# Performance work log

Measured on AMD Instinct MI355X. Metric: run time of the kernel, lower is better.

The kernel has to match this reference:

```python
import jax, jax.numpy as jnp
import numpy as np
from jax import lax

L1_DECAY = 1e-06


def _maxpool2(x):
    # NCHW 2x2 max pool, stride 2
    return lax.reduce_window(x, -jnp.inf, lax.max, (1, 1, 2, 2), (1, 1, 2, 2), 'VALID')


def _cnn(x, w1, b1, w2, b2, wo, bo):
    # x: [N,128,128] -> [N,64], z-score normalized over batch dim
    x = x[:, None]  # [N,1,128,128]
    dn = ('NCHW', 'OIHW', 'NCHW')
    x = lax.conv_general_dilated(x, w1, (1, 1), 'SAME', dimension_numbers=dn) + b1[None, :, None, None]
    x = _maxpool2(jax.nn.relu(x))  # [N,4,64,64]
    x = lax.conv_general_dilated(x, w2, (1, 1), 'SAME', dimension_numbers=dn) + b2[None, :, None, None]
    x = _maxpool2(jax.nn.relu(x))  # [N,8,32,32]
    x = x.reshape(x.shape[0], -1)  # [N,8192] (C,H,W order, as torch .view)
    x = x @ wo.T + bo  # [N,64]
    mean = x.mean(axis=0)
    std = x.std(axis=0, ddof=1)  # torch unbiased std
    return (x - mean) / std


def _interact(item, nbr):
    # item: [N,64]; nbr: [N,H,K,64]. dot-attention over K per node/hop.
    scores = jnp.einsum('nhkd,nd->nhk', nbr, item)
    attn = jax.nn.softmax(scores, axis=-1)
    return jnp.einsum('nhk,nhkd->nhd', attn, nbr)  # [N,H,64]


def setup_inputs() -> dict:
    key = jax.random.key(0)
    ks = jax.random.split(key, 16)
    B = 4096
    inp = {}
    inp['data'] = jax.random.randint(ks[0], (B, 3), 0, 76)
    inp['cell_nbr'] = jax.random.randint(ks[1], (76, 2, 128), 0, 15970)
    inp['drug_nbr'] = jax.random.randint(ks[2], (764, 2, 128), 0, 15970)
    inp['protein_table'] = jax.random.normal(ks[3], (15970, 64), jnp.float32)
    inp['cell_emb_pre'] = jax.random.normal(ks[4], (76, 128, 128), jnp.float32)
    inp['drug_emb_pre'] = jax.random.normal(ks[5], (764, 128, 128), jnp.float32)
    inp['conv1_w'] = 0.05 * jax.random.normal(ks[6], (4, 1, 3, 3), jnp.float32)
    inp['conv1_b'] = 0.05 * jax.random.normal(ks[7], (4,), jnp.float32)
    inp['conv2_w'] = 0.05 * jax.random.normal(ks[8], (8, 4, 3, 3), jnp.float32)
    inp['conv2_b'] = 0.05 * jax.random.normal(ks[9], (8,), jnp.float32)
    inp['out_w'] = 0.05 * jax.random.normal(ks[10], (64, 8192), jnp.float32)
    inp['out_b'] = 0.05 * jax.random.normal(ks[11], (64,), jnp.float32)
    inp['agg_w'] = 0.05 * jax.random.normal(ks[12], (64, 128), jnp.float32)
    inp['agg_b'] = 0.05 * jax.random.normal(ks[13], (64,), jnp.float32)
    inp['comb_w'] = 0.05 * jax.random.normal(ks[14], (64, 128), jnp.float32)
    return inp


def reference(data, cell_nbr, drug_nbr, protein_table, cell_emb_pre, drug_emb_pre,
              conv1_w, conv1_b, conv2_w, conv2_b, out_w, out_b, agg_w, agg_b, comb_w):
    cells, drug1, drug2 = data[:, 0], data[:, 1], data[:, 2]
    B = data.shape[0]

    # per-node neighbor embedding gather: [num, n_hop, K, 64]
    cell_nbr_emb = protein_table[cell_nbr]
    drug_nbr_emb = protein_table[drug_nbr]

    # CNN item embeddings from precomputed images
    cell_item = _cnn(cell_emb_pre, conv1_w, conv1_b, conv2_w, conv2_b, out_w, out_b)  # [76,64]
    drug_item = _cnn(drug_emb_pre, conv1_w, conv1_b, conv2_w, conv2_b, out_w, out_b)  # [764,64]

    # gather -> attend -> weighted sum, then concat hops and aggregate
    cell_i = _interact(cell_item, cell_nbr_emb).reshape(cell_item.shape[0], -1)  # [76,128]
    drug_i = _interact(drug_item, drug_nbr_emb).reshape(drug_item.shape[0], -1)  # [764,128]
    cell_emb = cell_i @ agg_w.T + agg_b  # [76,64]
    drug_emb = drug_i @ agg_w.T + agg_b  # [764,64]

    # batch gather, keep singleton dim 1 to match torch stacking of [1,64]
    ce = cell_emb[cells][:, None, :]   # [B,1,64]
    d1e = drug_emb[drug1][:, None, :]
    d2e = drug_emb[drug2][:, None, :]

    # therapy: transformation_matrix
    combined = jnp.concatenate([d1e, d2e], axis=2) @ comb_w.T  # [B,1,64]
    therapy = (combined * ce).sum(axis=2)  # [B,1]
    toxic = (d1e * d2e).sum(axis=2)        # [B,1]
    score = therapy - toxic

    # emb loss (faithful to source: neighbor lists are indexed on the BATCH dim by hop)
    cnl = cell_nbr_emb[cells]   # [B,2,128,64]
    dnl1 = drug_nbr_emb[drug1]
    dnl2 = drug_nbr_emb[drug2]
    sq = lambda t: jnp.sum(t * t)
    item_reg = (sq(ce) + sq(d1e) + sq(d2e)) / 2
    node_reg = jnp.float32(0.0)
    for hop in range(2):
        node_reg = node_reg + (sq(cnl[hop]) + sq(dnl1[hop]) + sq(dnl2[hop])) / 2
    emb_loss = L1_DECAY * (item_reg + node_reg) / B
    return score, emb_loss
```

## Files before the change

### kernel.cpp

```cpp
#include <hip/hip_runtime.h>
#include <hip/hip_bf16.h>
#include <math.h>

#define N_CELL 76
#define N_DRUG 764
#define N_ITEM 840
#define BATCH  4096

#define POOL2H_B 0u
#define POOL2L_B 13762560u
#define WHI_B    27525120u
#define WLO_B    28573696u
#define XFC_B    29622272u
#define ITEM_B   29837312u
#define EMB_B    30052352u
#define V_B      30267392u
#define LOSS_B   30306304u
#define CNT_B    30306368u
#define FRAG_B   30306432u

typedef short bh8 __attribute__((ext_vector_type(8)));
typedef short bh4 __attribute__((ext_vector_type(4)));
typedef float f32x4 __attribute__((ext_vector_type(4)));

static __device__ inline unsigned short f2bf(float f) {
  union { float f; unsigned u; } v; v.f = f;
  unsigned r = v.u + 0x7FFFu + ((v.u >> 16) & 1u);
  return (unsigned short)(r >> 16);
}
static __device__ inline float bf2f(unsigned short h) {
  union { unsigned u; float f; } v; v.u = ((unsigned)h) << 16;
  return v.f;
}
static __device__ inline unsigned short f2bf_lo(float f, unsigned short h) {
  union { float f; unsigned u; } a; a.f = f - bf2f(h);
  return (unsigned short)(a.u >> 16);
}
static __device__ inline unsigned cvtpk(float a, float b) {
  unsigned r;
  asm("v_cvt_pk_bf16_f32 %0, %1, %2" : "=v"(r) : "v"(a), "v"(b));
  return r;
}
static __device__ inline float fromu(unsigned u) {
  union { unsigned u; float f; } v; v.u = u; return v.f;
}
static __device__ inline unsigned asu(float f) {
  union { float f; unsigned u; } v; v.f = f; return v.u;
}

union BH8U { bh8 v; struct { bh4 lo, hi; } s; };

__global__ __launch_bounds__(64) void k_prep(
    const float* __restrict__ w1, const float* __restrict__ w2,
    const float* __restrict__ b2, bh8* __restrict__ ftab,
    float* __restrict__ loss, unsigned* __restrict__ cnt) {
  int lane = threadIdx.x & 63;
  int ml = lane & 15, q = lane >> 4;
  int oc = ml & 3, yv1 = (ml >> 2) & 1, hi = ml >> 3;
  bh8 BhE, BlE, BhO, BlO;
  {
    int kr = q - yv1;
    bool krok = (kr >= 0 && kr <= 2);
#pragma unroll
    for (int j = 0; j < 8; ++j) {
      float ve = 0.f, vo = 0.f;
      if (krok) {
        int kse = j - 3 - 2 * hi;
        int kso = j - 2 * hi;
        if (kse >= 0 && kse <= 2) ve = w1[oc * 9 + kr * 3 + kse];
        if (kso >= 0 && kso <= 2) vo = w1[oc * 9 + kr * 3 + kso];
      }
      unsigned short he = f2bf(ve), ho = f2bf(vo);
      BhE[j] = (short)he; BlE[j] = (short)f2bf_lo(ve, he);
      BhO[j] = (short)ho; BlO[j] = (short)f2bf_lo(vo, ho);
    }
  }
  int oc_b = ml & 7, yv2 = ml >> 3;
  bh8 Bh2[2], Bl2[2];
#pragma unroll
  for (int ch = 0; ch < 2; ++ch) {
#pragma unroll
    for (int j = 0; j < 8; ++j) {
      int kg = ch * 32 + q * 8 + j;
      float v = 0.f;
      if (kg < 48) {
        int r = kg / 12, rem = kg - r * 12;
        int ks = rem >> 2, ic = rem & 3;
        int kr = r - yv2;
        if (kr >= 0 && kr <= 2) v = w2[(oc_b * 4 + ic) * 9 + kr * 3 + ks];
      } else if (kg == 48) {
        v = b2[oc_b];
      }
      unsigned short h = f2bf(v);
      Bh2[ch][j] = (short)h;
      Bl2[ch][j] = (short)f2bf_lo(v, h);
    }
  }
  ftab[lane] = BhE;          ftab[64 + lane] = BlE;
  ftab[128 + lane] = BhO;    ftab[192 + lane] = BlO;
  ftab[256 + lane] = Bh2[0]; ftab[320 + lane] = Bl2[0];
  ftab[384 + lane] = Bh2[1]; ftab[448 + lane] = Bl2[1];
  if (lane == 0) { *loss = 0.f; *cnt = 0u; }
}

__global__ __launch_bounds__(512) void k_conv12(
    const float* __restrict__ cell_pre, const float* __restrict__ drug_pre,
    const float* __restrict__ b1, const float* __restrict__ out_w,
    const bh8* __restrict__ ftab,
    unsigned short* __restrict__ pool2h, unsigned short* __restrict__ pool2l,
    unsigned short* __restrict__ whi, unsigned short* __restrict__ wlo,
    float* __restrict__ xfc) {
  __shared__ unsigned short slh[38 * 34 * 4];
  __shared__ unsigned short sll[38 * 34 * 4];
  __shared__ unsigned short p1h[18 * 66 * 4];
  __shared__ unsigned short p1l[18 * 66 * 4];
  int n = blockIdx.y;
  int tid = threadIdx.x;
  if (n >= 840) {
    int cb = (n - 840) * 4 + blockIdx.x;
    int gid = cb * 512 + tid;
    for (int i = gid; i < 13440; i += 10240)
      ((float4*)xfc)[i] = make_float4(0.f, 0.f, 0.f, 0.f);
    for (int i = gid; i < 131072; i += 10240) {
      float4 v = ((const float4*)out_w)[i];
      unsigned h01 = cvtpk(v.x, v.y), h23 = cvtpk(v.z, v.w);
      float d0 = v.x - fromu(h01 << 16), d1 = v.y - fromu(h01 & 0xFFFF0000u);
      float d2 = v.z - fromu(h23 << 16), d3 = v.w - fromu(h23 & 0xFFFF0000u);
      uint2 hh; hh.x = h01; hh.y = h23;
      uint2 lw; lw.x = cvtpk(d0, d1); lw.y = cvtpk(d2, d3);
      ((uint2*)whi)[i] = hh;
      ((uint2*)wlo)[i] = lw;
    }
    return;
  }
  int qt = blockIdx.x;
  const float4* src = (const float4*)((n < N_CELL) ? (cell_pre + (size_t)n * 16384)
                                                   : (drug_pre + (size_t)(n - N_CELL) * 16384));
  for (int i = tid; i < 38 * 32; i += 512) {
    int lr = i >> 5, g = i & 31;
    int iy = qt * 32 - 3 + lr;
    float4 v = make_float4(0.f, 0.f, 0.f, 0.f);
    if (iy >= 0 && iy < 128) v = src[iy * 32 + g];
    unsigned h01 = cvtpk(v.x, v.y), h23 = cvtpk(v.z, v.w);
    unsigned l01 = (asu(v.x - fromu(h01 << 16)) >> 16) |
                   (asu(v.y - fromu(h01 & 0xFFFF0000u)) & 0xFFFF0000u);
    unsigned l23 = (asu(v.z - fromu(h23 << 16)) >> 16) |
                   (asu(v.w - fromu(h23 & 0xFFFF0000u)) & 0xFFFF0000u);
    uint2 hh; hh.x = h01; hh.y = h23;
    uint2 lw; lw.x = l01; lw.y = l23;
    ((uint2*)slh)[lr * 34 + g + 1] = hh;
    ((uint2*)sll)[lr * 34 + g + 1] = lw;
  }
  if (tid < 76) {
    int lr = tid >> 1, g = (tid & 1) ? 33 : 0;
    ushort4 z = make_ushort4(0, 0, 0, 0);
    ((ushort4*)slh)[lr * 34 + g] = z;
    ((ushort4*)sll)[lr * 34 + g] = z;
  }
  if (tid < 36) {
    int r = tid >> 1, c = (tid & 1) ? 65 : 0;
    ushort4 z = make_ushort4(0, 0, 0, 0);
    ((ushort4*)p1h)[r * 66 + c] = z;
    ((ushort4*)p1l)[r * 66 + c] = z;
  }
  int wv = tid >> 6;
  int lane = tid & 63;
  int ml = lane & 15, q = lane >> 4;
  int oc = ml & 3, yv1 = (ml >> 2) & 1, hi = ml >> 3;
  int oc_b = ml & 7, yv2 = ml >> 3;
  float bb = b1[oc];

  bh8 BhE = ftab[lane],        BlE = ftab[64 + lane];
  bh8 BhO = ftab[128 + lane],  BlO = ftab[192 + lane];
  bh8 Bh20 = ftab[256 + lane], Bl20 = ftab[320 + lane];
  bh8 Bh21 = ftab[384 + lane], Bl21 = ftab[448 + lane];

  int c0 = 2 * q, c1 = 2 * q + 1;
  int c2 = 8 + 2 * q, c3 = 9 + 2 * q;
  if (c2 > 11) { c2 = 8; c3 = 9; }
  int r0 = (c0 * 86) >> 8, s0 = c0 - 3 * r0;
  int r1 = (c1 * 86) >> 8, s1 = c1 - 3 * r1;
  int r2 = (c2 * 86) >> 8, s2 = c2 - 3 * r2;
  int r3 = (c3 * 86) >> 8, s3 = c3 - 3 * r3;
  int x2 = (wv & 3) << 4;
  int off0 = r0 * 66 + x2 + ml + s0;
  int off1 = r1 * 66 + x2 + ml + s1;
  int off2 = r2 * 66 + x2 + ml + s2;
  int off3 = r3 * 66 + x2 + ml + s3;
  __syncthreads();

  int x0 = (wv & 1) * 16;
  int g1 = wv >> 1;
  int rbase = (g1 < 2) ? g1 * 5 : 10 + (g1 - 2) * 4;
  int rcnt  = (g1 < 2) ? 5 : 4;
  int Lb = x0 + ml;
  const bh4* lh4 = (const bh4*)slh;
  const bh4* ll4 = (const bh4*)sll;
#pragma unroll 1
  for (int ii = 0; ii < rcnt; ++ii) {
    int i = rbase + ii;
    int base = (2 * i + q) * 34 + Lb;
    bh4 g0h = lh4[base], g1h = lh4[base + 1], g2h = lh4[base + 2];
    bh4 g0l = ll4[base], g1l = ll4[base + 1], g2l = ll4[base + 2];
    BH8U aeh, ael, aoh, aol;
    aeh.s.lo = g0h; aeh.s.hi = g1h;
    ael.s.lo = g0l; ael.s.hi = g1l;
    aoh.s.lo = g1h; aoh.s.hi = g2h;
    aol.s.lo = g1l; aol.s.hi = g2l;
    f32x4 de = {0.f, 0.f, 0.f, 0.f}, dd = de;
    de = __builtin_amdgcn_mfma_f32_16x16x32_bf16(aeh.v, BhE, de, 0, 0, 0);
    de = __builtin_amdgcn_mfma_f32_16x16x32_bf16(aeh.v, BlE, de, 0, 0, 0);
    de = __builtin_amdgcn_mfma_f32_16x16x32_bf16(ael.v, BhE, de, 0, 0, 0);
    dd = __builtin_amdgcn_mfma_f32_16x16x32_bf16(aoh.v, BhO, dd, 0, 0, 0);
    dd = __builtin_amdgcn_mfma_f32_16x16x32_bf16(aoh.v, BlO, dd, 0, 0, 0);
    dd = __builtin_amdgcn_mfma_f32_16x16x32_bf16(aol.v, BhO, dd, 0, 0, 0);
    int pr = qt * 16 - 1 + i;
    bool inr = (pr >= 0 && pr < 64);
    float t, t2, v0, v1, v2, v3;
    t = fmaxf(de[0], dd[0]); t2 = __shfl_xor(t, 4); v0 = fmaxf(fmaxf(t, t2) + bb, 0.f);
    t = fmaxf(de[1], dd[1]); t2 = __shfl_xor(t, 4); v1 = fmaxf(fmaxf(t, t2) + bb, 0.f);
    t = fmaxf(de[2], dd[2]); t2 = __shfl_xor(t, 4); v2 = fmaxf(fmaxf(t, t2) + bb, 0.f);
    t = fmaxf(de[3], dd[3]); t2 = __shfl_xor(t, 4); v3 = fmaxf(fmaxf(t, t2) + bb, 0.f);
    if (yv1 == 0) {
      if (!inr) { v0 = 0.f; v1 = 0.f; v2 = 0.f; v3 = 0.f; }
      unsigned pk01 = cvtpk(v0, v1), pk23 = cvtpk(v2, v3);
      unsigned l0 = asu(v0 - fromu(pk01 << 16)) >> 16;
      unsigned l1 = asu(v1 - fromu(pk01 & 0xFFFF0000u)) >> 16;
      unsigned l2 = asu(v2 - fromu(pk23 << 16)) >> 16;
      unsigned l3 = asu(v3 - fromu(pk23 & 0xFFFF0000u)) >> 16;
      int idx = (i * 66 + 2 * (x0 + q * 4) + hi + 1) * 4 + oc;
      p1h[idx] = (unsigned short)pk01;              p1l[idx] = (unsigned short)l0;
      p1h[idx + 8] = (unsigned short)(pk01 >> 16);  p1l[idx + 8] = (unsigned short)l1;
      p1h[idx + 16] = (unsigned short)pk23;         p1l[idx + 16] = (unsigned short)l2;
      p1h[idx + 24] = (unsigned short)(pk23 >> 16); p1l[idx + 24] = (unsigned short)l3;
    }
  }
  __syncthreads();

  int rp0 = (wv >> 2) * 4;
  const bh4* ph4 = (const bh4*)p1h;
  const bh4* pl4 = (const bh4*)p1l;
#pragma unroll 1
  for (int rr = 0; rr < 4; ++rr) {
    int rp = rp0 + rr;
    int base2 = 2 * rp * 66;
    BH8U ah0, al0, ah1, al1;
    ah0.s.lo = ph4[base2 + off0]; ah0.s.hi = ph4[base2 + off1];
    al0.s.lo = pl4[base2 + off0]; al0.s.hi = pl4[base2 + off1];
    if (q < 2) {
      ah1.s.lo = ph4[base2 + off2]; ah1.s.hi = ph4[base2 + off3];
      al1.s.lo = pl4[base2 + off2]; al1.s.hi = pl4[base2 + off3];
    } else {
#pragma unroll
      for (int j = 0; j < 8; ++j) { ah1.v[j] = 0; al1.v[j] = 0; }
      if (q == 2) ah1.v[0] = (short)0x3F80;
    }
    f32x4 accA = {0.f, 0.f, 0.f, 0.f}, accB = accA;
    accA = __builtin_amdgcn_mfma_f32_16x16x32_bf16(ah0.v, Bh20, accA, 0, 0, 0);
    accA = __builtin_amdgcn_mfma_f32_16x16x32_bf16(ah0.v, Bl20, accA, 0, 0, 0);
    accA = __builtin_amdgcn_mfma_f32_16x16x32_bf16(al0.v, Bh20, accA, 0, 0, 0);
    accB = __builtin_amdgcn_mfma_f32_16x16x32_bf16(ah1.v, Bh21, accB, 0, 0, 0);
    accB = __builtin_amdgcn_mfma_f32_16x16x32_bf16(ah1.v, Bl21, accB, 0, 0, 0);
    accB = __builtin_amdgcn_mfma_f32_16x16x32_bf16(al1.v, Bh21, accB, 0, 0, 0);
    float d0 = accA[0] + accB[0], d1 = accA[1] + accB[1];
    float d2 = accA[2] + accB[2], d3 = accA[3] + accB[3];
    float m0 = fmaxf(d0, d1), m1 = fmaxf(d2, d3);
    float o0 = __shfl_xor(m0, 8), o1 = __shfl_xor(m1, 8);
    m0 = fmaxf(fmaxf(m0, o0), 0.f);
    m1 = fmaxf(fmaxf(m1, o1), 0.f);
    if (yv2 == 0) {
      unsigned pk = cvtpk(m0, m1);
      float e0 = m0 - fromu(pk << 16), e1 = m1 - fromu(pk & 0xFFFF0000u);
      unsigned lw = cvtpk(e0, e1);
      int PR = qt * 8 + rp;
      unsigned ui = (unsigned)n * 4096u + (unsigned)oc_b * 512u +
                    (unsigned)PR * 16u + (unsigned)(x2 >> 2) + (unsigned)q;
      ((unsigned*)pool2h)[ui] = pk;
      ((unsigned*)pool2l)[ui] = lw;
    }
  }
}

__global__ __launch_bounds__(512) void k_fc(
    const unsigned short* __restrict__ pool2h, const unsigned short* __restrict__ pool2l,
    const unsigned short* __restrict__ whi, const unsigned short* __restrict__ wlo,
    float* __restrict__ xfc) {
  __shared__ float buf[8][1104];
  int mt = blockIdx.x, kc4 = blockIdx.y;
  int tid = threadIdx.x;
  int wv = tid >> 6;
  int lane = tid & 63;
  int ml = lane & 15, q = lane >> 4;
  int row = mt * 16 + ml; if (row > N_ITEM - 1) row = N_ITEM - 1;
  size_t k0 = ((size_t)kc4 * 8 + wv) * 256 + q * 8;
  const bh8* Ah = (const bh8*)(pool2h + (size_t)row * 8192 + k0);
  const bh8* Al = (const bh8*)(pool2l + (size_t)row * 8192 + k0);
  const bh8* Bh[4], * Bl[4];
#pragma unroll
  for (int nb = 0; nb < 4; ++nb) {
    Bh[nb] = (const bh8*)(whi + (size_t)(nb * 16 + ml) * 8192 + k0);
    Bl[nb] = (const bh8*)(wlo + (size_t)(nb * 16 + ml) * 8192 + k0);
  }
  f32x4 acc[4];
#pragma unroll
  for (int nb = 0; nb < 4; ++nb) acc[nb] = (f32x4){0.f, 0.f, 0.f, 0.f};
#pragma unroll
  for (int st = 0; st < 8; ++st) {
    bh8 ah = Ah[st * 4], al = Al[st * 4];
#pragma unroll
    for (int nb = 0; nb < 4; ++nb) {
      bh8 bhv = Bh[nb][st * 4], blv = Bl[nb][st * 4];
      acc[nb] = __builtin_amdgcn_mfma_f32_16x16x32_bf16(ah, bhv, acc[nb], 0, 0, 0);
      acc[nb] = __builtin_amdgcn_mfma_f32_16x16x32_bf16(ah, blv, acc[nb], 0, 0, 0);
      acc[nb] = __builtin_amdgcn_mfma_f32_16x16x32_bf16(al, bhv, acc[nb], 0, 0, 0);
    }
  }
  {
    float* bw = &buf[wv][lane * 17];
#pragma unroll
    for (int nb = 0; nb < 4; ++nb)
#pragma unroll
      for (int r = 0; r < 4; ++r) bw[nb * 4 + r] = acc[nb][r];
  }
  __syncthreads();
#pragma unroll
  for (int su = 0; su < 2; ++su) {
    int s = tid + su * 512;
    int ln = s >> 4, j = s & 15;
    int phys = ln * 17 + j;
    float v = buf[0][phys] + buf[1][phys] + buf[2][phys] + buf[3][phys] +
              buf[4][phys] + buf[5][phys] + buf[6][phys] + buf[7][phys];
    int nb = j >> 2, r = j & 3;
    int mml = ln & 15, mq = ln >> 4;
    int mr = mt * 16 + mq * 4 + r;
    if (mr < N_ITEM) atomicAdd(xfc + (size_t)mr * 64 + nb * 16 + mml, v);
  }
}

__global__ __launch_bounds__(256) void k_norm(
    const float* __restrict__ xfc, float* __restrict__ item) {
  __shared__ float red[256];
  int grp = blockIdx.x >> 6;
  int o = blockIdx.x & 63;
  int base = grp ? N_CELL : 0;
  int N = grp ? N_DRUG : N_CELL;
  int tid = threadIdx.x;
  float s = 0.f;
  for (int i = tid; i < N; i += 256) s += xfc[(size_t)(base + i) * 64 + o];
  red[tid] = s; __syncthreads();
  for (int w = 128; w > 0; w >>= 1) { if (tid < w) red[tid] += red[tid + w]; __syncthreads(); }
  float mean = red[0] / (float)N;
  __syncthreads();
  float sq = 0.f;
  for (int i = tid; i < N; i += 256) {
    float d = xfc[(size_t)(base + i) * 64 + o] - mean;
    sq += d * d;
  }
  red[tid] = sq; __syncthreads();
  for (int w = 128; w > 0; w >>= 1) { if (tid < w) red[tid] += red[tid + w]; __syncthreads(); }
  float inv_std = 1.f / sqrtf(red[0] / (float)(N - 1));
  for (int i = tid; i < N; i += 256)
    item[(size_t)(base + i) * 64 + o] = (xfc[(size_t)(base + i) * 64 + o] - mean) * inv_std;
}

__global__ __launch_bounds__(512) void k_interact(
    const int* __restrict__ cell_nbr, const int* __restrict__ drug_nbr,
    const float* __restrict__ protein, const float* __restrict__ item,
    const float* __restrict__ agg_w, const float* __restrict__ agg_b,
    const float* __restrict__ comb_w, float* __restrict__ emb,
    float* __restrict__ V) {
  __shared__ float pb[2][128 * 65];
  __shared__ float item_s[64];
  __shared__ float sc[2][128];
  __shared__ float hop_out[128];
  __shared__ float red[512];
  __shared__ float emb_f[64];
  int n = blockIdx.x;
  int tid = threadIdx.x;
  int ht = tid >> 8;
  int t = tid & 255;
  const int* nbr = (n < N_CELL) ? (cell_nbr + (size_t)n * 256)
                                : (drug_nbr + (size_t)(n - N_CELL) * 256);
  if (tid < 64) item_s[tid] = item[(size_t)n * 64 + tid];
  __syncthreads();
  for (int e = t; e < 8192; e += 256) {
    int k = e >> 6, d = e & 63;
    int idx = nbr[ht * 128 + k];
    pb[ht][k * 65 + d] = protein[(size_t)idx * 64 + d];
  }
  __syncthreads();
  {
    int k = t >> 1, halfd = t & 1;
    int d0 = halfd * 32;
    float p = 0.f;
#pragma unroll
    for (int d = 0; d < 32; ++d) p += item_s[d0 + d] * pb[ht][k * 65 + d0 + d];
    p += __shfl_xor(p, 1);
    if (halfd == 0) sc[ht][k] = p;
  }
  __syncthreads();
  if (t < 64) {
    float a = sc[ht][t], b = sc[ht][t + 64];
    float m = fmaxf(a, b);
#pragma unroll
    for (int off = 32; off > 0; off >>= 1) m = fmaxf(m, __shfl_xor(m, off));
    float e0 = __expf(a - m), e1 = __expf(b - m);
    float s = e0 + e1;
#pragma unroll
    for (int off = 32; off > 0; off >>= 1) s += __shfl_xor(s, off);
    float inv = 1.f / s;
    sc[ht][t] = e0 * inv; sc[ht][t + 64] = e1 * inv;
  }
  __syncthreads();
  {
    int d = t & 63, kq = t >> 6;
    float p = 0.f;
#pragma unroll
    for (int k = 0; k < 32; ++k) {
      int kk = kq * 32 + k;
      p += sc[ht][kk] * pb[ht][kk * 65 + d];
    }
    red[tid] = p;
  }
  __syncthreads();
  if (t < 64)
    hop_out[ht * 64 + t] = red[ht * 256 + t] + red[ht * 256 + t + 64] +
                           red[ht * 256 + t + 128] + red[ht * 256 + t + 192];
  __syncthreads();
  {
    int o = tid & 63, jq = tid >> 6;
    float p = 0.f;
#pragma unroll
    for (int j = 0; j < 16; ++j) {
      int jj = jq * 16 + j;
      p += hop_out[jj] * agg_w[(size_t)o * 128 + jj];
    }
    red[tid] = p;
  }
  __syncthreads();
  if (tid < 64) {
    float ev = red[tid] + red[tid + 64] + red[tid + 128] + red[tid + 192] +
               red[tid + 256] + red[tid + 320] + red[tid + 384] + red[tid + 448] +
               agg_b[tid];
    emb[(size_t)n * 64 + tid] = ev;
    emb_f[tid] = ev;
  }
  if (n < N_CELL) {
    __syncthreads();
    if (tid < 128) {
      float s = 0.f;
#pragma unroll
      for (int o = 0; o < 64; ++o) s += comb_w[(size_t)o * 128 + tid] * emb_f[o];
      V[(size_t)n * 128 + tid] = s;
    }
  }
}

__global__ __launch_bounds__(512) void k_scoreall(
    const int* __restrict__ data, const int* __restrict__ cell_nbr,
    const int* __restrict__ drug_nbr, const float* __restrict__ protein,
    const float* __restrict__ emb, const float* __restrict__ V,
    float* __restrict__ out, float* __restrict__ loss, unsigned* __restrict__ cnt) {
  __shared__ float red[8];
  int bx = blockIdx.x;
  int tid = threadIdx.x;
  int lane = tid & 63;
  int wv = tid >> 6;
  float part = 0.f;
  if (bx < 64) {
    int b0 = bx * 64 + wv * 8;
#pragma unroll 1
    for (int i = 0; i < 8; ++i) {
      int b = b0 + i;
      int c = data[b * 3 + 0], d1 = data[b * 3 + 1], d2 = data[b * 3 + 2];
      float ce = emb[(size_t)c * 64 + lane];
      float e1 = emb[(size_t)(N_CELL + d1) * 64 + lane];
      float e2 = emb[(size_t)(N_CELL + d2) * 64 + lane];
      float v1 = V[(size_t)c * 128 + lane];
      float v2 = V[(size_t)c * 128 + 64 + lane];
      float s = e1 * v1 + e2 * v2 - e1 * e2;
      part += ce * ce + e1 * e1 + e2 * e2;
#pragma unroll
      for (int off = 32; off > 0; off >>= 1) s += __shfl_xor(s, off);
      if (lane == 0) out[b] = s;
    }
  } else {
    int j = bx - 64;
    int hop = j / 3, which = j % 3;
    int row = data[hop * 3 + which];
    const int* nbr = (which == 0) ? (cell_nbr + (size_t)row * 256)
                                  : (drug_nbr + (size_t)row * 256);
    for (int e = tid; e < 16384; e += 512) {
      int k = e >> 6, d = e & 63;
      float v = protein[(size_t)nbr[k] * 64 + d];
      part += v * v;
    }
  }
#pragma unroll
  for (int off = 32; off > 0; off >>= 1) part += __shfl_xor(part, off);
  if (lane == 0) red[wv] = part;
  __syncthreads();
  if (tid == 0) {
    float s = red[0] + red[1] + red[2] + red[3] + red[4] + red[5] + red[6] + red[7];
    atomicAdd(loss, 0.5f * s);
    __threadfence();
    unsigned old = atomicAdd(cnt, 1u);
    if (old == gridDim.x - 1) {
      float L = atomicAdd(loss, 0.f);
      out[BATCH] = L * (1e-6f / 4096.f);
    }
  }
}

extern "C" void kernel_launch(void* const* d_in, const int* in_sizes, int n_in,
                              void* d_out, int out_size, void* d_ws, size_t ws_size,
                              hipStream_t stream) {
  const int*   data      = (const int*)d_in[0];
  const int*   cell_nbr  = (const int*)d_in[1];
  const int*   drug_nbr  = (const int*)d_in[2];
  const float* protein   = (const float*)d_in[3];
  const float* cell_pre  = (const float*)d_in[4];
  const float* drug_pre  = (const float*)d_in[5];
  const float* w1        = (const float*)d_in[6];
  const float* b1        = (const float*)d_in[7];
  const float* w2        = (const float*)d_in[8];
  const float* b2        = (const float*)d_in[9];
  const float* out_w     = (const float*)d_in[10];
  const float* agg_w     = (const float*)d_in[12];
  const float* agg_b     = (const float*)d_in[13];
  const float* comb_w    = (const float*)d_in[14];
  float* out = (float*)d_out;
  char* base = (char*)d_ws;
  unsigned short* pool2h  = (unsigned short*)(base + POOL2H_B);
  unsigned short* pool2l  = (unsigned short*)(base + POOL2L_B);
  unsigned short* whi     = (unsigned short*)(base + WHI_B);
  unsigned short* wlo     = (unsigned short*)(base + WLO_B);
  float* xfc              = (float*)(base + XFC_B);
  float* item             = (float*)(base + ITEM_B);
  float* emb              = (float*)(base + EMB_B);
  float* V                = (float*)(base + V_B);
  float* loss             = (float*)(base + LOSS_B);
  unsigned* cnt           = (unsigned*)(base + CNT_B);
  bh8* ftab               = (bh8*)(base + FRAG_B);

  k_prep<<<1, 64, 0, stream>>>(w1, w2, b2, ftab, loss, cnt);
  k_conv12<<<dim3(4, 845), 512, 0, stream>>>(cell_pre, drug_pre, b1, out_w, ftab,
                                             pool2h, pool2l, whi, wlo, xfc);
  k_fc<<<dim3(53, 4), 512, 0, stream>>>(pool2h, pool2l, whi, wlo, xfc);
  k_norm<<<128, 256, 0, stream>>>(xfc, item);
  k_interact<<<840, 512, 0, stream>>>(cell_nbr, drug_nbr, protein, item, agg_w, agg_b,
                                      comb_w, emb, V);
  k_scoreall<<<70, 512, 0, stream>>>(data, cell_nbr, drug_nbr, protein, emb, V, out, loss, cnt);
}
```

Before: 211.2 us.

## Process all four row-quarters per block with register-prefetched next halo tile

The conv kernel now launches one block per item instead of four, looping over the four 32-row quarters inside the block. While conv2 of the current quarter runs, the global loads for the next quarter's input tile are issued into registers and written to shared memory afterwards, so load latency overlaps compute. This cuts the grid from 3380 to 845 blocks, which reduces parallelism and may hurt latency hiding, but it removes per-block launch overhead and one redundant halo reload. It adds extra barriers and register pressure from the prefetched float4 values.

```diff
diff --git a/kernel.cpp b/kernel.cpp
--- a/kernel.cpp
+++ b/kernel.cpp
@@ -114,14 +114,13 @@
   __shared__ unsigned short sll[38 * 34 * 4];
   __shared__ unsigned short p1h[18 * 66 * 4];
   __shared__ unsigned short p1l[18 * 66 * 4];
-  int n = blockIdx.y;
+  int n = blockIdx.x;
   int tid = threadIdx.x;
   if (n >= 840) {
-    int cb = (n - 840) * 4 + blockIdx.x;
-    int gid = cb * 512 + tid;
-    for (int i = gid; i < 13440; i += 10240)
+    int gid = (n - 840) * 512 + tid;
+    for (int i = gid; i < 13440; i += 2560)
       ((float4*)xfc)[i] = make_float4(0.f, 0.f, 0.f, 0.f);
-    for (int i = gid; i < 131072; i += 10240) {
+    for (int i = gid; i < 131072; i += 2560) {
       float4 v = ((const float4*)out_w)[i];
       unsigned h01 = cvtpk(v.x, v.y), h23 = cvtpk(v.z, v.w);
       float d0 = v.x - fromu(h01 << 16), d1 = v.y - fromu(h01 & 0xFFFF0000u);
@@ -133,24 +132,8 @@
     }
     return;
   }
-  int qt = blockIdx.x;
   const float4* src = (const float4*)((n < N_CELL) ? (cell_pre + (size_t)n * 16384)
                                                    : (drug_pre + (size_t)(n - N_CELL) * 16384));
-  for (int i = tid; i < 38 * 32; i += 512) {
-    int lr = i >> 5, g = i & 31;
-    int iy = qt * 32 - 3 + lr;
-    float4 v = make_float4(0.f, 0.f, 0.f, 0.f);
-    if (iy >= 0 && iy < 128) v = src[iy * 32 + g];
-    unsigned h01 = cvtpk(v.x, v.y), h23 = cvtpk(v.z, v.w);
-    unsigned l01 = (asu(v.x - fromu(h01 << 16)) >> 16) |
-                   (asu(v.y - fromu(h01 & 0xFFFF0000u)) & 0xFFFF0000u);
-    unsigned l23 = (asu(v.z - fromu(h23 << 16)) >> 16) |
-                   (asu(v.w - fromu(h23 & 0xFFFF0000u)) & 0xFFFF0000u);
-    uint2 hh; hh.x = h01; hh.y = h23;
-    uint2 lw; lw.x = l01; lw.y = l23;
-    ((uint2*)slh)[lr * 34 + g + 1] = hh;
-    ((uint2*)sll)[lr * 34 + g + 1] = lw;
-  }
   if (tid < 76) {
     int lr = tid >> 1, g = (tid & 1) ? 33 : 0;
     ushort4 z = make_ushort4(0, 0, 0, 0);
@@ -187,96 +170,157 @@
   int off1 = r1 * 66 + x2 + ml + s1;
   int off2 = r2 * 66 + x2 + ml + s2;
   int off3 = r3 * 66 + x2 + ml + s3;
-  __syncthreads();
-
   int x0 = (wv & 1) * 16;
   int g1 = wv >> 1;
   int rbase = (g1 < 2) ? g1 * 5 : 10 + (g1 - 2) * 4;
   int rcnt  = (g1 < 2) ? 5 : 4;
   int Lb = x0 + ml;
+  int rp0 = (wv >> 2) * 4;
   const bh4* lh4 = (const bh4*)slh;
   const bh4* ll4 = (const bh4*)sll;
-#pragma unroll 1
-  for (int ii = 0; ii < rcnt; ++ii) {
-    int i = rbase + ii;
-    int base = (2 * i + q) * 34 + Lb;
-    bh4 g0h = lh4[base], g1h = lh4[base + 1], g2h = lh4[base + 2];
-    bh4 g0l = ll4[base], g1l = ll4[base + 1], g2l = ll4[base + 2];
-    BH8U aeh, ael, aoh, aol;
-    aeh.s.lo = g0h; aeh.s.hi = g1h;
-    ael.s.lo = g0l; ael.s.hi = g1l;
-    aoh.s.lo = g1h; aoh.s.hi = g2h;
-    aol.s.lo = g1l; aol.s.hi = g2l;
-    f32x4 de = {0.f, 0.f, 0.f, 0.f}, dd = de;
-    de = __builtin_amdgcn_mfma_f32_16x16x32_bf16(aeh.v, BhE, de, 0, 0, 0);
-    de = __builtin_amdgcn_mfma_f32_16x16x32_bf16(aeh.v, BlE, de, 0, 0, 0);
-    de = __builtin_amdgcn_mfma_f32_16x16x32_bf16(ael.v, BhE, de, 0, 0, 0);
-    dd = __builtin_amdgcn_mfma_f32_16x16x32_bf16(aoh.v, BhO, dd, 0, 0, 0);
-    dd = __builtin_amdgcn_mfma_f32_16x16x32_bf16(aoh.v, BlO, dd, 0, 0, 0);
-    dd = __builtin_amdgcn_mfma_f32_16x16x32_bf16(aol.v, BhO, dd, 0, 0, 0);
-    int pr = qt * 16 - 1 + i;
-    bool inr = (pr >= 0 && pr < 64);
-    float t, t2, v0, v1, v2, v3;
-    t = fmaxf(de[0], dd[0]); t2 = __shfl_xor(t, 4); v0 = fmaxf(fmaxf(t, t2) + bb, 0.f);
-    t = fmaxf(de[1], dd[1]); t2 = __shfl_xor(t, 4); v1 = fmaxf(fmaxf(t, t2) + bb, 0.f);
-    t = fmaxf(de[2], dd[2]); t2 = __shfl_xor(t, 4); v2 = fmaxf(fmaxf(t, t2) + bb, 0.f);
-    t = fmaxf(de[3], dd[3]); t2 = __shfl_xor(t, 4); v3 = fmaxf(fmaxf(t, t2) + bb, 0.f);
-    if (yv1 == 0) {
-      if (!inr) { v0 = 0.f; v1 = 0.f; v2 = 0.f; v3 = 0.f; }
-      unsigned pk01 = cvtpk(v0, v1), pk23 = cvtpk(v2, v3);
-      unsigned l0 = asu(v0 - fromu(pk01 << 16)) >> 16;
-      unsigned l1 = asu(v1 - fromu(pk01 & 0xFFFF0000u)) >> 16;
-      unsigned l2 = asu(v2 - fromu(pk23 << 16)) >> 16;
-      unsigned l3 = asu(v3 - fromu(pk23 & 0xFFFF0000u)) >> 16;
-      int idx = (i * 66 + 2 * (x0 + q * 4) + hi + 1) * 4 + oc;
-      p1h[idx] = (unsigned short)pk01;              p1l[idx] = (unsigned short)l0;
-      p1h[idx + 8] = (unsigned short)(pk01 >> 16);  p1l[idx + 8] = (unsigned short)l1;
-      p1h[idx + 16] = (unsigned short)pk23;         p1l[idx + 16] = (unsigned short)l2;
-      p1h[idx + 24] = (unsigned short)(pk23 >> 16); p1l[idx + 24] = (unsigned short)l3;
-    }
-  }
-  __syncthreads();
-
-  int rp0 = (wv >> 2) * 4;
   const bh4* ph4 = (const bh4*)p1h;
   const bh4* pl4 = (const bh4*)p1l;
+  int si0 = tid, si1 = tid + 512, si2 = tid + 1024;
+  bool sk2 = (si2 < 1216);
+
+  for (int i = tid; i < 1216; i += 512) {
+    int lr = i >> 5, g = i & 31;
+    int iy = -3 + lr;
+    float4 v = make_float4(0.f, 0.f, 0.f, 0.f);
+    if (iy >= 0 && iy < 128) v = src[iy * 32 + g];
+    unsigned h01 = cvtpk(v.x, v.y), h23 = cvtpk(v.z, v.w);
+    unsigned l01 = (asu(v.x - fromu(h01 << 16)) >> 16) |
+                   (asu(v.y - fromu(h01 & 0xFFFF0000u)) & 0xFFFF0000u);
+    unsigned l23 = (asu(v.z - fromu(h23 << 16)) >> 16) |
+                   (asu(v.w - fromu(h23 & 0xFFFF0000u)) & 0xFFFF0000u);
+    uint2 hh; hh.x = h01; hh.y = h23;
+    uint2 lw; lw.x = l01; lw.y = l23;
+    ((uint2*)slh)[lr * 34 + g + 1] = hh;
+    ((uint2*)sll)[lr * 34 + g + 1] = lw;
+  }
+  __syncthreads();
+
 #pragma unroll 1
-  for (int rr = 0; rr < 4; ++rr) {
-    int rp = rp0 + rr;
-    int base2 = 2 * rp * 66;
-    BH8U ah0, al0, ah1, al1;
-    ah0.s.lo = ph4[base2 + off0]; ah0.s.hi = ph4[base2 + off1];
-    al0.s.lo = pl4[base2 + off0]; al0.s.hi = pl4[base2 + off1];
-    if (q < 2) {
-      ah1.s.lo = ph4[base2 + off2]; ah1.s.hi = ph4[base2 + off3];
-      al1.s.lo = pl4[base2 + off2]; al1.s.hi = pl4[base2 + off3];
-    } else {
-#pragma unroll
-      for (int j = 0; j < 8; ++j) { ah1.v[j] = 0; al1.v[j] = 0; }
-      if (q == 2) ah1.v[0] = (short)0x3F80;
-    }
-    f32x4 accA = {0.f, 0.f, 0.f, 0.f}, accB = accA;
-    accA = __builtin_amdgcn_mfma_f32_16x16x32_bf16(ah0.v, Bh20, accA, 0, 0, 0);
-    accA = __builtin_amdgcn_mfma_f32_16x16x32_bf16(ah0.v, Bl20, accA, 0, 0, 0);
-    accA = __builtin_amdgcn_mfma_f32_16x16x32_bf16(al0.v, Bh20, accA, 0, 0, 0);
-    accB = __builtin_amdgcn_mfma_f32_16x16x32_bf16(ah1.v, Bh21, accB, 0, 0, 0);
-    accB = __builtin_amdgcn_mfma_f32_16x16x32_bf16(ah1.v, Bl21, accB, 0, 0, 0);
-    accB = __builtin_amdgcn_mfma_f32_16x16x32_bf16(al1.v, Bh21, accB, 0, 0, 0);
-    float d0 = accA[0] + accB[0], d1 = accA[1] + accB[1];
-    float d2 = accA[2] + accB[2], d3 = accA[3] + accB[3];
-    float m0 = fmaxf(d0, d1), m1 = fmaxf(d2, d3);
-    float o0 = __shfl_xor(m0, 8), o1 = __shfl_xor(m1, 8);
-    m0 = fmaxf(fmaxf(m0, o0), 0.f);
-    m1 = fmaxf(fmaxf(m1, o1), 0.f);
-    if (yv2 == 0) {
-      unsigned pk = cvtpk(m0, m1);
-      float e0 = m0 - fromu(pk << 16), e1 = m1 - fromu(pk & 0xFFFF0000u);
-      unsigned lw = cvtpk(e0, e1);
-      int PR = qt * 8 + rp;
-      unsigned ui = (unsigned)n * 4096u + (unsigned)oc_b * 512u +
-                    (unsigned)PR * 16u + (unsigned)(x2 >> 2) + (unsigned)q;
-      ((unsigned*)pool2h)[ui] = pk;
-      ((unsigned*)pool2l)[ui] = lw;
+  for (int qt = 0; qt < 4; ++qt) {
+#pragma unroll 1
+    for (int ii = 0; ii < rcnt; ++ii) {
+      int i = rbase + ii;
+      int base = (2 * i + q) * 34 + Lb;
+      bh4 g0h = lh4[base], g1h = lh4[base + 1], g2h = lh4[base + 2];
+      bh4 g0l = ll4[base], g1l = ll4[base + 1], g2l = ll4[base + 2];
+      BH8U aeh, ael, aoh, aol;
+      aeh.s.lo = g0h; aeh.s.hi = g1h;
+      ael.s.lo = g0l; ael.s.hi = g1l;
+      aoh.s.lo = g1h; aoh.s.hi = g2h;
+      aol.s.lo = g1l; aol.s.hi = g2l;
+      f32x4 de = {0.f, 0.f, 0.f, 0.f}, dd = de;
+      de = __builtin_amdgcn_mfma_f32_16x16x32_bf16(aeh.v, BhE, de, 0, 0, 0);
+      de = __builtin_amdgcn_mfma_f32_16x16x32_bf16(aeh.v, BlE, de, 0, 0, 0);
+      de = __builtin_amdgcn_mfma_f32_16x16x32_bf16(ael.v, BhE, de, 0, 0, 0);
+      dd = __builtin_amdgcn_mfma_f32_16x16x32_bf16(aoh.v, BhO, dd, 0, 0, 0);
+      dd = __builtin_amdgcn_mfma_f32_16x16x32_bf16(aoh.v, BlO, dd, 0, 0, 0);
+      dd = __builtin_amdgcn_mfma_f32_16x16x32_bf16(aol.v, BhO, dd, 0, 0, 0);
+      int pr = qt * 16 - 1 + i;
+      bool inr = (pr >= 0 && pr < 64);
+      float t, t2, v0, v1, v2, v3;
+      t = fmaxf(de[0], dd[0]); t2 = __shfl_xor(t, 4); v0 = fmaxf(fmaxf(t, t2) + bb, 0.f);
+      t = fmaxf(de[1], dd[1]); t2 = __shfl_xor(t, 4); v1 = fmaxf(fmaxf(t, t2) + bb, 0.f);
+      t = fmaxf(de[2], dd[2]); t2 = __shfl_xor(t, 4); v2 = fmaxf(fmaxf(t, t2) + bb, 0.f);
+      t = fmaxf(de[3], dd[3]); t2 = __shfl_xor(t, 4); v3 = fmaxf(fmaxf(t, t2) + bb, 0.f);
+      if (yv1 == 0) {
+        if (!inr) { v0 = 0.f; v1 = 0.f; v2 = 0.f; v3 = 0.f; }
+        unsigned pk01 = cvtpk(v0, v1), pk23 = cvtpk(v2, v3);
+        unsigned l0 = asu(v0 - fromu(pk01 << 16)) >> 16;
+        unsigned l1 = asu(v1 - fromu(pk01 & 0xFFFF0000u)) >> 16;
+        unsigned l2 = asu(v2 - fromu(pk23 << 16)) >> 16;
+        unsigned l3 = asu(v3 - fromu(pk23 & 0xFFFF0000u)) >> 16;
+        int idx = (i * 66 + 2 * (x0 + q * 4) + hi + 1) * 4 + oc;
+        p1h[idx] = (unsigned short)pk01;              p1l[idx] = (unsigned short)l0;
+        p1h[idx + 8] = (unsigned short)(pk01 >> 16);  p1l[idx + 8] = (unsigned short)l1;
+        p1h[idx + 16] = (unsigned short)pk23;         p1l[idx + 16] = (unsigned short)l2;
+        p1h[idx + 24] = (unsigned short)(pk23 >> 16); p1l[idx + 24] = (unsigned short)l3;
+      }
+    }
+    __syncthreads();
+
+    float4 stv0, stv1, stv2;
+    if (qt < 3) {
+      int cy0 = (qt + 1) * 32 - 3;
+      {
+        int iy = cy0 + (si0 >> 5);
+        stv0 = (iy >= 0 && iy < 128) ? src[iy * 32 + (si0 & 31)]
+                                     : make_float4(0.f, 0.f, 0.f, 0.f);
+      }
+      {
+        int iy = cy0 + (si1 >> 5);
+        stv1 = (iy >= 0 && iy < 128) ? src[iy * 32 + (si1 & 31)]
+                                     : make_float4(0.f, 0.f, 0.f, 0.f);
+      }
+      if (sk2) {
+        int iy = cy0 + (si2 >> 5);
+        stv2 = (iy >= 0 && iy < 128) ? src[iy * 32 + (si2 & 31)]
+                                     : make_float4(0.f, 0.f, 0.f, 0.f);
+      }
+    }
+
+#pragma unroll 1
+    for (int rr = 0; rr < 4; ++rr) {
+      int rp = rp0 + rr;
+      int base2 = 2 * rp * 66;
+      BH8U ah0, al0, ah1, al1;
+      ah0.s.lo = ph4[base2 + off0]; ah0.s.hi = ph4[base2 + off1];
+      al0.s.lo = pl4[base2 + off0]; al0.s.hi = pl4[base2 + off1];
+      if (q < 2) {
+        ah1.s.lo = ph4[base2 + off2]; ah1.s.hi = ph4[base2 + off3];
+        al1.s.lo = pl4[base2 + off2]; al1.s.hi = pl4[base2 + off3];
+      } else {
+#pragma unroll
+        for (int j = 0; j < 8; ++j) { ah1.v[j] = 0; al1.v[j] = 0; }
+        if (q == 2) ah1.v[0] = (short)0x3F80;
+      }
+      f32x4 accA = {0.f, 0.f, 0.f, 0.f}, accB = accA;
+      accA = __builtin_amdgcn_mfma_f32_16x16x32_bf16(ah0.v, Bh20, accA, 0, 0, 0);
+      accA = __builtin_amdgcn_mfma_f32_16x16x32_bf16(ah0.v, Bl20, accA, 0, 0, 0);
+      accA = __builtin_amdgcn_mfma_f32_16x16x32_bf16(al0.v, Bh20, accA, 0, 0, 0);
+      accB = __builtin_amdgcn_mfma_f32_16x16x32_bf16(ah1.v, Bh21, accB, 0, 0, 0);
+      accB = __builtin_amdgcn_mfma_f32_16x16x32_bf16(ah1.v, Bl21, accB, 0, 0, 0);
+      accB = __builtin_amdgcn_mfma_f32_16x16x32_bf16(al1.v, Bh21, accB, 0, 0, 0);
+      float d0 = accA[0] + accB[0], d1 = accA[1] + accB[1];
+      float d2 = accA[2] + accB[2], d3 = accA[3] + accB[3];
+      float m0 = fmaxf(d0, d1), m1 = fmaxf(d2, d3);
+      float o0 = __shfl_xor(m0, 8), o1 = __shfl_xor(m1, 8);
+      m0 = fmaxf(fmaxf(m0, o0), 0.f);
+      m1 = fmaxf(fmaxf(m1, o1), 0.f);
+      if (yv2 == 0) {
+        unsigned pk = cvtpk(m0, m1);
+        float e0 = m0 - fromu(pk << 16), e1 = m1 - fromu(pk & 0xFFFF0000u);
+        unsigned lw = cvtpk(e0, e1);
+        int PR = qt * 8 + rp;
+        unsigned ui = (unsigned)n * 4096u + (unsigned)oc_b * 512u +
+                      (unsigned)PR * 16u + (unsigned)(x2 >> 2) + (unsigned)q;
+        ((unsigned*)pool2h)[ui] = pk;
+        ((unsigned*)pool2l)[ui] = lw;
+      }
+    }
+
+    if (qt < 3) {
+#pragma unroll
+      for (int it = 0; it < 3; ++it) {
+        if (it == 2 && !sk2) break;
+        float4 v = (it == 0) ? stv0 : (it == 1) ? stv1 : stv2;
+        int i = (it == 0) ? si0 : (it == 1) ? si1 : si2;
+        int lr = i >> 5, g = i & 31;
+        unsigned h01 = cvtpk(v.x, v.y), h23 = cvtpk(v.z, v.w);
+        unsigned l01 = (asu(v.x - fromu(h01 << 16)) >> 16) |
+                       (asu(v.y - fromu(h01 & 0xFFFF0000u)) & 0xFFFF0000u);
+        unsigned l23 = (asu(v.z - fromu(h23 << 16)) >> 16) |
+                       (asu(v.w - fromu(h23 & 0xFFFF0000u)) & 0xFFFF0000u);
+        uint2 hh; hh.x = h01; hh.y = h23;
+        uint2 lw; lw.x = l01; lw.y = l23;
+        ((uint2*)slh)[lr * 34 + g + 1] = hh;
+        ((uint2*)sll)[lr * 34 + g + 1] = lw;
+      }
+      __syncthreads();
     }
   }
 }
@@ -544,8 +588,8 @@
   bh8* ftab               = (bh8*)(base + FRAG_B);
 
   k_prep<<<1, 64, 0, stream>>>(w1, w2, b2, ftab, loss, cnt);
-  k_conv12<<<dim3(4, 845), 512, 0, stream>>>(cell_pre, drug_pre, b1, out_w, ftab,
-                                             pool2h, pool2l, whi, wlo, xfc);
+  k_conv12<<<845, 512, 0, stream>>>(cell_pre, drug_pre, b1, out_w, ftab,
+                                    pool2h, pool2l, whi, wlo, xfc);
   k_fc<<<dim3(53, 4), 512, 0, stream>>>(pool2h, pool2l, whi, wlo, xfc);
   k_norm<<<128, 256, 0, stream>>>(xfc, item);
   k_interact<<<840, 512, 0, stream>>>(cell_nbr, drug_nbr, protein, item, agg_w, agg_b,
```

Result: slower. 218.8 us (+3.6%).
